# Kernel optimization log

Measured on AMD Instinct MI355X. Metric: run time of the kernel, lower is better.

## Reference

```python
import jax, jax.numpy as jnp
import numpy as np

N_ENTITIES = 500000
N_RELATIONS = 200
EMBED_DIM = 128
RELATION_DIM = 128  # must equal EMBED_DIM for the reshape in calculate_score
BATCH = 16384
KG_L2_LAMBDA = 1e-5


def _xavier_uniform(key, shape):
    fan_in, fan_out = shape[0], shape[1]
    limit = float(np.sqrt(6.0 / (fan_in + fan_out)))
    return jax.random.uniform(key, shape, jnp.float32, -limit, limit)


def setup_inputs() -> dict:
    key = jax.random.key(0)
    k1, k2, k3, k4, k5, k6 = jax.random.split(key, 6)
    entity_embed = _xavier_uniform(k1, (N_ENTITIES, EMBED_DIM))
    relation_embed = _xavier_uniform(k2, (N_RELATIONS, RELATION_DIM * EMBED_DIM))
    h = jax.random.randint(k3, (BATCH,), 0, N_ENTITIES, dtype=jnp.int64)
    r = jax.random.randint(k4, (BATCH,), 0, N_RELATIONS, dtype=jnp.int64)
    pos_t = jax.random.randint(k5, (BATCH,), 0, N_ENTITIES, dtype=jnp.int64)
    neg_t = jax.random.randint(k6, (BATCH,), 0, N_ENTITIES, dtype=jnp.int64)
    return {"h": h, "r": r, "pos_t": pos_t, "neg_t": neg_t,
            "entity_embed": entity_embed, "relation_embed": relation_embed}


def _l2_loss_mean(x):
    # mean over batch of sum(x^2, dim=1) / 2
    return jnp.mean(jnp.sum(x * x, axis=1) / 2.0)


def _score(h_e, t_e, r_mat):
    # r_mat: (B, relation_dim, embed_dim); tr = r @ t : (B, embed_dim)
    tr = jnp.einsum('bde,be->bd', r_mat, t_e)
    return -jnp.sum(h_e * tr, axis=-1)  # (B,)


def reference(h, r, pos_t, neg_t, entity_embed, relation_embed):
    r_embed = relation_embed[r]                     # (B, R*D)
    head_embed = entity_embed[h]                    # (B, D)
    tail_pos_embed = entity_embed[pos_t]            # (B, D)
    tail_neg_embed = entity_embed[neg_t]            # (B, D)
    r_mat = r_embed.reshape(-1, RELATION_DIM, EMBED_DIM)
    pos_score = _score(head_embed, tail_pos_embed, r_mat)
    neg_score = _score(head_embed, tail_neg_embed, r_mat)
    triplet_loss = jnp.mean(-jax.nn.log_sigmoid(neg_score - pos_score))
    l2_loss = (_l2_loss_mean(head_embed) + _l2_loss_mean(r_embed)
               + _l2_loss_mean(tail_pos_embed) + _l2_loss_mean(tail_neg_embed))
    return triplet_loss + KG_L2_LAMBDA * l2_loss
```

## Files before the change

### kernel.cpp

```cpp
#include <hip/hip_runtime.h>
#include <math.h>

#define BATCH 16384
#define EDIM 128
#define RD (EDIM * EDIM)
#define NREL 200
#define SPLIT 4
#define NBLK (NREL * SPLIT)
#define NTHR 256
#define QUARTER (BATCH / SPLIT)
#define NJ (QUARTER / NTHR)
#define EB 8
#define LISTCAP 256


__device__ __forceinline__ int load_idx(const void* p, int b, int is64) {
    if (is64) return (int)((const long long*)p)[b];
    return ((const int*)p)[b];
}

__global__ __launch_bounds__(NTHR) void rescal_kernel(
    const void* __restrict__ hI, const void* __restrict__ rI,
    const void* __restrict__ pI, const void* __restrict__ nI,
    const float* __restrict__ ent, const float* __restrict__ rel,
    float* __restrict__ csum) {
    const int t = threadIdx.x;
    const int bid0 = blockIdx.x;
    const int xcd = bid0 & 7;
    const int slot = bid0 >> 3;
    const int rid = xcd + 8 * (slot >> 2);
    const int qtr = slot & 3;
    const int lane = t & 63;
    const int wave = t >> 6;
    const int c2 = lane * 2;

    __shared__ unsigned short list[LISTCAP];
    __shared__ unsigned int wtj[NJ][4];
    __shared__ unsigned int um4[4];
    __shared__ float wsum[4];

    unsigned int o = ((const unsigned int*)hI)[2 * t + 1] |
                     ((const unsigned int*)rI)[2 * t + 1] |
                     ((const unsigned int*)pI)[2 * t + 1] |
                     ((const unsigned int*)nI)[2 * t + 1];
#pragma unroll
    for (int off = 32; off; off >>= 1) o |= __shfl_xor(o, off, 64);
    if (lane == 0) um4[wave] = o;
    __syncthreads();
    const int is64 = ((um4[0] | um4[1] | um4[2] | um4[3]) == 0u) ? 1 : 0;

    const int qbase = qtr * QUARTER;
    unsigned long long bal[NJ];
#pragma unroll
    for (int j = 0; j < NJ; ++j) {
        const int rr = load_idx(rI, qbase + j * NTHR + t, is64);
        bal[j] = __ballot(rr == rid);
        if (lane == 0) wtj[j][wave] = (unsigned int)__popcll(bal[j]);
    }
    __syncthreads();
    int cnt;
    {
        unsigned int run = 0;
        const unsigned long long ltmask = (lane == 63) ? ~0ull >> 1
                                                       : (1ull << lane) - 1ull;
#pragma unroll
        for (int j = 0; j < NJ; ++j) {
            unsigned int wpre = 0, tj = 0;
#pragma unroll
            for (int w = 0; w < 4; ++w) {
                const unsigned int v = wtj[j][w];
                tj += v;
                wpre += (w < wave) ? v : 0;
            }
            if ((bal[j] >> lane) & 1ull) {
                const unsigned int rank =
                    run + wpre + (unsigned int)__popcll(bal[j] & ltmask);
                if (rank < LISTCAP) list[rank] = (unsigned short)(j * NTHR + t);
            }
            run += tj;
        }
        cnt = (int)run;
        if (cnt > LISTCAP) cnt = LISTCAP;
    }
    __syncthreads();

    const int per_wave = (cnt + 3) >> 2;
    int lo = wave * per_wave;
    int hi = (wave + 1) * per_wave;
    if (lo > cnt) lo = cnt;
    if (hi > cnt) hi = cnt;

    const float* Rg = rel + (size_t)rid * RD;
    float lsum = 0.f;
    float r2w = 0.f;

    for (int e0 = lo; e0 < hi; e0 += EB) {
        int bidx[EB];
        const float* hrow[EB];
#pragma unroll
        for (int i = 0; i < EB; ++i) {
            int e = e0 + i;
            if (e >= hi) e = hi - 1;
            int b = qbase + (int)list[e];
            b = __builtin_amdgcn_readfirstlane(b);
            bidx[i] = b;
            int hix = load_idx(hI, b, is64);
            hix = __builtin_amdgcn_readfirstlane(hix);
            hrow[i] = ent + (size_t)hix * EDIM;
        }

        float2 acc[EB];
#pragma unroll
        for (int i = 0; i < EB; ++i) acc[i] = make_float2(0.f, 0.f);
        float r2p = 0.f;
#pragma unroll 4
        for (int db = 0; db < 32; ++db) {
            float4 hv0 = *(const float4*)(hrow[0] + db * 4);
            float4 hv1 = *(const float4*)(hrow[1] + db * 4);
            float4 hv2 = *(const float4*)(hrow[2] + db * 4);
            float4 hv3 = *(const float4*)(hrow[3] + db * 4);
            float4 hv4 = *(const float4*)(hrow[4] + db * 4);
            float4 hv5 = *(const float4*)(hrow[5] + db * 4);
            float4 hv6 = *(const float4*)(hrow[6] + db * 4);
            float4 hv7 = *(const float4*)(hrow[7] + db * 4);
#pragma unroll
            for (int jj = 0; jj < 4; ++jj) {
                const int d = db * 4 + jj;
                const float2 r2v = *(const float2*)(Rg + d * EDIM + c2);
                r2p = fmaf(r2v.x, r2v.x, fmaf(r2v.y, r2v.y, r2p));
                const float h0 = (jj == 0) ? hv0.x : (jj == 1) ? hv0.y : (jj == 2) ? hv0.z : hv0.w;
                const float h1 = (jj == 0) ? hv1.x : (jj == 1) ? hv1.y : (jj == 2) ? hv1.z : hv1.w;
                const float h2 = (jj == 0) ? hv2.x : (jj == 1) ? hv2.y : (jj == 2) ? hv2.z : hv2.w;
                const float h3 = (jj == 0) ? hv3.x : (jj == 1) ? hv3.y : (jj == 2) ? hv3.z : hv3.w;
                const float h4 = (jj == 0) ? hv4.x : (jj == 1) ? hv4.y : (jj == 2) ? hv4.z : hv4.w;
                const float h5 = (jj == 0) ? hv5.x : (jj == 1) ? hv5.y : (jj == 2) ? hv5.z : hv5.w;
                const float h6 = (jj == 0) ? hv6.x : (jj == 1) ? hv6.y : (jj == 2) ? hv6.z : hv6.w;
                const float h7 = (jj == 0) ? hv7.x : (jj == 1) ? hv7.y : (jj == 2) ? hv7.z : hv7.w;
                acc[0].x = fmaf(r2v.x, h0, acc[0].x); acc[0].y = fmaf(r2v.y, h0, acc[0].y);
                acc[1].x = fmaf(r2v.x, h1, acc[1].x); acc[1].y = fmaf(r2v.y, h1, acc[1].y);
                acc[2].x = fmaf(r2v.x, h2, acc[2].x); acc[2].y = fmaf(r2v.y, h2, acc[2].y);
                acc[3].x = fmaf(r2v.x, h3, acc[3].x); acc[3].y = fmaf(r2v.y, h3, acc[3].y);
                acc[4].x = fmaf(r2v.x, h4, acc[4].x); acc[4].y = fmaf(r2v.y, h4, acc[4].y);
                acc[5].x = fmaf(r2v.x, h5, acc[5].x); acc[5].y = fmaf(r2v.y, h5, acc[5].y);
                acc[6].x = fmaf(r2v.x, h6, acc[6].x); acc[6].y = fmaf(r2v.y, h6, acc[6].y);
                acc[7].x = fmaf(r2v.x, h7, acc[7].x); acc[7].y = fmaf(r2v.y, h7, acc[7].y);
            }
        }
#pragma unroll
        for (int off = 32; off; off >>= 1) r2p += __shfl_xor(r2p, off, 64);
        r2w = r2p;

#pragma unroll
        for (int i = 0; i < EB; ++i) {
            const int b = bidx[i];
            int pi = __builtin_amdgcn_readfirstlane(load_idx(pI, b, is64));
            int ni = __builtin_amdgcn_readfirstlane(load_idx(nI, b, is64));
            const float2 hv2 = *(const float2*)(hrow[i] + c2);
            const float2 tp2 = *(const float2*)(ent + (size_t)pi * EDIM + c2);
            const float2 tn2 = *(const float2*)(ent + (size_t)ni * EDIM + c2);
            float dp = acc[i].x * tp2.x + acc[i].y * tp2.y;
            float dn = acc[i].x * tn2.x + acc[i].y * tn2.y;
            float e2 = hv2.x * hv2.x + hv2.y * hv2.y + tp2.x * tp2.x + tp2.y * tp2.y +
                       tn2.x * tn2.x + tn2.y * tn2.y;
#pragma unroll
            for (int off = 32; off; off >>= 1) {
                dp += __shfl_xor(dp, off, 64);
                dn += __shfl_xor(dn, off, 64);
                e2 += __shfl_xor(e2, off, 64);
            }
            if (lane == 0 && (e0 + i) < hi) {
                const float x = dn - dp;
                const float spl = (x > 0.f) ? (x + log1pf(expf(-x))) : log1pf(expf(x));
                lsum += spl + 1e-5f * 0.5f * (e2 + r2w);
            }
        }
    }

    if (lane == 0) wsum[wave] = lsum;
    __syncthreads();
    if (t == 0) csum[bid0] = wsum[0] + wsum[1] + wsum[2] + wsum[3];
}

__global__ __launch_bounds__(NTHR) void reduce_kernel(const float* __restrict__ csum,
                                                      float* __restrict__ out) {
    const int t = threadIdx.x;
    float a = 0.f;
    for (int i = t; i < NBLK; i += NTHR) a += csum[i];
#pragma unroll
    for (int off = 32; off; off >>= 1) a += __shfl_down(a, off, 64);
    __shared__ float sm[4];
    if ((t & 63) == 0) sm[t >> 6] = a;
    __syncthreads();
    if (t == 0) out[0] = (sm[0] + sm[1] + sm[2] + sm[3]) * (1.0f / (float)BATCH);
}

extern "C" void kernel_launch(void* const* d_in, const int* in_sizes, int n_in,
                              void* d_out, int out_size, void* d_ws, size_t ws_size,
                              hipStream_t stream) {
    const void* h = d_in[0];
    const void* r = d_in[1];
    const void* pt = d_in[2];
    const void* nt = d_in[3];
    const float* ent = (const float*)d_in[4];
    const float* rel = (const float*)d_in[5];
    float* csum = (float*)d_ws;

    rescal_kernel<<<NBLK, NTHR, 0, stream>>>(h, r, pt, nt, ent, rel, csum);
    reduce_kernel<<<1, NTHR, 0, stream>>>(csum, (float*)d_out);
}
```

Measured before the change: 54.09 us.

## Split relation rows across waves and fuse final reduction via last-block atomic

Work inside a block is now split across the four waves by the d dimension of the relation matrix (32 rows per wave) instead of by batch entries. Each wave computes partial r@h products for groups of 16 entries, and the partials are summed through shared memory. This cuts each wave's relation-matrix reads to a quarter but adds two block barriers per group. The separate reduce kernel is replaced by a last-block-done atomic counter, reset by a memset, so one kernel launch is removed in exchange for a memset and fences.

```diff
diff --git a/kernel.cpp b/kernel.cpp
--- a/kernel.cpp
+++ b/kernel.cpp
@@ -10,7 +10,7 @@
 #define NTHR 256
 #define QUARTER (BATCH / SPLIT)
 #define NJ (QUARTER / NTHR)
-#define EB 8
+#define GE 16
 #define LISTCAP 256
 
 
@@ -23,7 +23,7 @@
     const void* __restrict__ hI, const void* __restrict__ rI,
     const void* __restrict__ pI, const void* __restrict__ nI,
     const float* __restrict__ ent, const float* __restrict__ rel,
-    float* __restrict__ csum) {
+    float* __restrict__ ws, float* __restrict__ out) {
     const int t = threadIdx.x;
     const int bid0 = blockIdx.x;
     const int xcd = bid0 & 7;
@@ -34,10 +34,12 @@
     const int wave = t >> 6;
     const int c2 = lane * 2;
 
+    __shared__ float uw[4][GE][EDIM];
     __shared__ unsigned short list[LISTCAP];
     __shared__ unsigned int wtj[NJ][4];
     __shared__ unsigned int um4[4];
-    __shared__ float wsum[4];
+    __shared__ float wred[4], wsum[4];
+    __shared__ int s_last;
 
     unsigned int o = ((const unsigned int*)hI)[2 * t + 1] |
                      ((const unsigned int*)rI)[2 * t + 1] |
@@ -84,23 +86,18 @@
     }
     __syncthreads();
 
-    const int per_wave = (cnt + 3) >> 2;
-    int lo = wave * per_wave;
-    int hi = (wave + 1) * per_wave;
-    if (lo > cnt) lo = cnt;
-    if (hi > cnt) hi = cnt;
-
     const float* Rg = rel + (size_t)rid * RD;
+    const int dlo = wave * 32;
     float lsum = 0.f;
-    float r2w = 0.f;
-
-    for (int e0 = lo; e0 < hi; e0 += EB) {
-        int bidx[EB];
-        const float* hrow[EB];
-#pragma unroll
-        for (int i = 0; i < EB; ++i) {
-            int e = e0 + i;
-            if (e >= hi) e = hi - 1;
+    float r2sum = 0.f;
+
+    for (int g0 = 0; g0 < cnt; g0 += GE) {
+        int bidx[GE];
+        const float* hrow[GE];
+#pragma unroll
+        for (int i = 0; i < GE; ++i) {
+            int e = g0 + i;
+            if (e >= cnt) e = cnt - 1;
             int b = qbase + (int)list[e];
             b = __builtin_amdgcn_readfirstlane(b);
             bidx[i] = b;
@@ -109,57 +106,52 @@
             hrow[i] = ent + (size_t)hix * EDIM;
         }
 
-        float2 acc[EB];
-#pragma unroll
-        for (int i = 0; i < EB; ++i) acc[i] = make_float2(0.f, 0.f);
+        float2 acc[GE];
+#pragma unroll
+        for (int i = 0; i < GE; ++i) acc[i] = make_float2(0.f, 0.f);
         float r2p = 0.f;
 #pragma unroll 4
-        for (int db = 0; db < 32; ++db) {
-            float4 hv0 = *(const float4*)(hrow[0] + db * 4);
-            float4 hv1 = *(const float4*)(hrow[1] + db * 4);
-            float4 hv2 = *(const float4*)(hrow[2] + db * 4);
-            float4 hv3 = *(const float4*)(hrow[3] + db * 4);
-            float4 hv4 = *(const float4*)(hrow[4] + db * 4);
-            float4 hv5 = *(const float4*)(hrow[5] + db * 4);
-            float4 hv6 = *(const float4*)(hrow[6] + db * 4);
-            float4 hv7 = *(const float4*)(hrow[7] + db * 4);
-#pragma unroll
-            for (int jj = 0; jj < 4; ++jj) {
-                const int d = db * 4 + jj;
-                const float2 r2v = *(const float2*)(Rg + d * EDIM + c2);
-                r2p = fmaf(r2v.x, r2v.x, fmaf(r2v.y, r2v.y, r2p));
-                const float h0 = (jj == 0) ? hv0.x : (jj == 1) ? hv0.y : (jj == 2) ? hv0.z : hv0.w;
-                const float h1 = (jj == 0) ? hv1.x : (jj == 1) ? hv1.y : (jj == 2) ? hv1.z : hv1.w;
-                const float h2 = (jj == 0) ? hv2.x : (jj == 1) ? hv2.y : (jj == 2) ? hv2.z : hv2.w;
-                const float h3 = (jj == 0) ? hv3.x : (jj == 1) ? hv3.y : (jj == 2) ? hv3.z : hv3.w;
-                const float h4 = (jj == 0) ? hv4.x : (jj == 1) ? hv4.y : (jj == 2) ? hv4.z : hv4.w;
-                const float h5 = (jj == 0) ? hv5.x : (jj == 1) ? hv5.y : (jj == 2) ? hv5.z : hv5.w;
-                const float h6 = (jj == 0) ? hv6.x : (jj == 1) ? hv6.y : (jj == 2) ? hv6.z : hv6.w;
-                const float h7 = (jj == 0) ? hv7.x : (jj == 1) ? hv7.y : (jj == 2) ? hv7.z : hv7.w;
-                acc[0].x = fmaf(r2v.x, h0, acc[0].x); acc[0].y = fmaf(r2v.y, h0, acc[0].y);
-                acc[1].x = fmaf(r2v.x, h1, acc[1].x); acc[1].y = fmaf(r2v.y, h1, acc[1].y);
-                acc[2].x = fmaf(r2v.x, h2, acc[2].x); acc[2].y = fmaf(r2v.y, h2, acc[2].y);
-                acc[3].x = fmaf(r2v.x, h3, acc[3].x); acc[3].y = fmaf(r2v.y, h3, acc[3].y);
-                acc[4].x = fmaf(r2v.x, h4, acc[4].x); acc[4].y = fmaf(r2v.y, h4, acc[4].y);
-                acc[5].x = fmaf(r2v.x, h5, acc[5].x); acc[5].y = fmaf(r2v.y, h5, acc[5].y);
-                acc[6].x = fmaf(r2v.x, h6, acc[6].x); acc[6].y = fmaf(r2v.y, h6, acc[6].y);
-                acc[7].x = fmaf(r2v.x, h7, acc[7].x); acc[7].y = fmaf(r2v.y, h7, acc[7].y);
-            }
-        }
-#pragma unroll
-        for (int off = 32; off; off >>= 1) r2p += __shfl_xor(r2p, off, 64);
-        r2w = r2p;
-
-#pragma unroll
-        for (int i = 0; i < EB; ++i) {
+        for (int db = 0; db < 16; ++db) {
+            const int d0 = dlo + db * 2;
+            const float2 ra = *(const float2*)(Rg + d0 * EDIM + c2);
+            const float2 rb = *(const float2*)(Rg + (d0 + 1) * EDIM + c2);
+            r2p = fmaf(ra.x, ra.x, fmaf(ra.y, ra.y, fmaf(rb.x, rb.x, fmaf(rb.y, rb.y, r2p))));
+#pragma unroll
+            for (int i = 0; i < GE; ++i) {
+                const float2 hd = *(const float2*)(hrow[i] + d0);
+                acc[i].x = fmaf(ra.x, hd.x, acc[i].x);
+                acc[i].y = fmaf(ra.y, hd.x, acc[i].y);
+                acc[i].x = fmaf(rb.x, hd.y, acc[i].x);
+                acc[i].y = fmaf(rb.y, hd.y, acc[i].y);
+            }
+        }
+#pragma unroll
+        for (int i = 0; i < GE; ++i) *(float2*)&uw[wave][i][c2] = acc[i];
+        if (g0 == 0) {
+#pragma unroll
+            for (int off = 32; off; off >>= 1) r2p += __shfl_xor(r2p, off, 64);
+            if (lane == 0) wred[wave] = r2p;
+        }
+        __syncthreads();
+        if (g0 == 0) r2sum = wred[0] + wred[1] + wred[2] + wred[3];
+
+#pragma unroll
+        for (int q = 0; q < 4; ++q) {
+            const int i = wave * 4 + q;
+            const float2 v0 = *(const float2*)&uw[0][i][c2];
+            const float2 v1 = *(const float2*)&uw[1][i][c2];
+            const float2 v2 = *(const float2*)&uw[2][i][c2];
+            const float2 v3 = *(const float2*)&uw[3][i][c2];
+            const float ux = v0.x + v1.x + v2.x + v3.x;
+            const float uy = v0.y + v1.y + v2.y + v3.y;
             const int b = bidx[i];
-            int pi = __builtin_amdgcn_readfirstlane(load_idx(pI, b, is64));
-            int ni = __builtin_amdgcn_readfirstlane(load_idx(nI, b, is64));
+            const int pi = __builtin_amdgcn_readfirstlane(load_idx(pI, b, is64));
+            const int ni = __builtin_amdgcn_readfirstlane(load_idx(nI, b, is64));
             const float2 hv2 = *(const float2*)(hrow[i] + c2);
             const float2 tp2 = *(const float2*)(ent + (size_t)pi * EDIM + c2);
             const float2 tn2 = *(const float2*)(ent + (size_t)ni * EDIM + c2);
-            float dp = acc[i].x * tp2.x + acc[i].y * tp2.y;
-            float dn = acc[i].x * tn2.x + acc[i].y * tn2.y;
+            float dp = ux * tp2.x + uy * tp2.y;
+            float dn = ux * tn2.x + uy * tn2.y;
             float e2 = hv2.x * hv2.x + hv2.y * hv2.y + tp2.x * tp2.x + tp2.y * tp2.y +
                        tn2.x * tn2.x + tn2.y * tn2.y;
 #pragma unroll
@@ -168,30 +160,36 @@
                 dn += __shfl_xor(dn, off, 64);
                 e2 += __shfl_xor(e2, off, 64);
             }
-            if (lane == 0 && (e0 + i) < hi) {
+            if (lane == 0 && (g0 + i) < cnt) {
                 const float x = dn - dp;
                 const float spl = (x > 0.f) ? (x + log1pf(expf(-x))) : log1pf(expf(x));
-                lsum += spl + 1e-5f * 0.5f * (e2 + r2w);
-            }
-        }
+                lsum += spl + 1e-5f * 0.5f * (e2 + r2sum);
+            }
+        }
+        __syncthreads();
     }
 
     if (lane == 0) wsum[wave] = lsum;
     __syncthreads();
-    if (t == 0) csum[bid0] = wsum[0] + wsum[1] + wsum[2] + wsum[3];
-}
-
-__global__ __launch_bounds__(NTHR) void reduce_kernel(const float* __restrict__ csum,
-                                                      float* __restrict__ out) {
-    const int t = threadIdx.x;
-    float a = 0.f;
-    for (int i = t; i < NBLK; i += NTHR) a += csum[i];
-#pragma unroll
-    for (int off = 32; off; off >>= 1) a += __shfl_down(a, off, 64);
-    __shared__ float sm[4];
-    if ((t & 63) == 0) sm[t >> 6] = a;
-    __syncthreads();
-    if (t == 0) out[0] = (sm[0] + sm[1] + sm[2] + sm[3]) * (1.0f / (float)BATCH);
+    if (t == 0) {
+        ws[bid0] = wsum[0] + wsum[1] + wsum[2] + wsum[3];
+        __threadfence();
+        unsigned int old = atomicAdd((unsigned int*)(ws + 1024), 1u);
+        s_last = (old == (unsigned int)(NBLK - 1)) ? 1 : 0;
+    }
+    __syncthreads();
+    if (s_last) {
+        __threadfence();
+        float a = 0.f;
+        for (int i = t; i < NBLK; i += NTHR)
+            a += __hip_atomic_load(&ws[i], __ATOMIC_ACQUIRE, __HIP_MEMORY_SCOPE_AGENT);
+#pragma unroll
+        for (int off = 32; off; off >>= 1) a += __shfl_down(a, off, 64);
+        if (lane == 0) wsum[wave] = a;
+        __syncthreads();
+        if (t == 0)
+            out[0] = (wsum[0] + wsum[1] + wsum[2] + wsum[3]) * (1.0f / (float)BATCH);
+    }
 }
 
 extern "C" void kernel_launch(void* const* d_in, const int* in_sizes, int n_in,
@@ -203,8 +201,9 @@
     const void* nt = d_in[3];
     const float* ent = (const float*)d_in[4];
     const float* rel = (const float*)d_in[5];
-    float* csum = (float*)d_ws;
-
-    rescal_kernel<<<NBLK, NTHR, 0, stream>>>(h, r, pt, nt, ent, rel, csum);
-    reduce_kernel<<<1, NTHR, 0, stream>>>(csum, (float*)d_out);
+
+    hipMemsetAsync((void*)((char*)d_ws + 1024 * sizeof(float)), 0,
+                   sizeof(unsigned int), stream);
+    rescal_kernel<<<NBLK, NTHR, 0, stream>>>(h, r, pt, nt, ent, rel,
+                                             (float*)d_ws, (float*)d_out);
 }
```

New measurement: 126.6 us. +134.1%, slower.

## Split each relation across eight blocks and fuse final reduction via last-block atomic

Applied to the files above, without the earlier changes.

Doubles the per-relation batch split from 4 to 8 blocks (1600 blocks total) with a smaller entity batch of 4 and a smaller per-block list, which adds parallelism and lowers register pressure. The tail-embedding loads are hoisted ahead of the matvec loop so their latency overlaps it. The separate reduce kernel is removed: a last-block-done atomic counter now does the final sum inside the main kernel, at the cost of an extra memset launch. Each relation matrix is now re-read by twice as many blocks, and a smaller LISTCAP raises the risk of truncation if a relation's count exceeds 128 per piece.

```diff
diff --git a/kernel.cpp b/kernel.cpp
--- a/kernel.cpp
+++ b/kernel.cpp
@@ -5,13 +5,13 @@
 #define EDIM 128
 #define RD (EDIM * EDIM)
 #define NREL 200
-#define SPLIT 4
+#define SPLIT 8
 #define NBLK (NREL * SPLIT)
 #define NTHR 256
-#define QUARTER (BATCH / SPLIT)
-#define NJ (QUARTER / NTHR)
-#define EB 8
-#define LISTCAP 256
+#define PIECE (BATCH / SPLIT)
+#define NJ (PIECE / NTHR)
+#define EB 4
+#define LISTCAP 128
 
 
 __device__ __forceinline__ int load_idx(const void* p, int b, int is64) {
@@ -23,13 +23,13 @@
     const void* __restrict__ hI, const void* __restrict__ rI,
     const void* __restrict__ pI, const void* __restrict__ nI,
     const float* __restrict__ ent, const float* __restrict__ rel,
-    float* __restrict__ csum) {
+    float* __restrict__ ws, float* __restrict__ out) {
     const int t = threadIdx.x;
     const int bid0 = blockIdx.x;
     const int xcd = bid0 & 7;
     const int slot = bid0 >> 3;
-    const int rid = xcd + 8 * (slot >> 2);
-    const int qtr = slot & 3;
+    const int rid = xcd + 8 * (slot >> 3);
+    const int piece = slot & 7;
     const int lane = t & 63;
     const int wave = t >> 6;
     const int c2 = lane * 2;
@@ -38,6 +38,7 @@
     __shared__ unsigned int wtj[NJ][4];
     __shared__ unsigned int um4[4];
     __shared__ float wsum[4];
+    __shared__ int s_last;
 
     unsigned int o = ((const unsigned int*)hI)[2 * t + 1] |
                      ((const unsigned int*)rI)[2 * t + 1] |
@@ -49,7 +50,7 @@
     __syncthreads();
     const int is64 = ((um4[0] | um4[1] | um4[2] | um4[3]) == 0u) ? 1 : 0;
 
-    const int qbase = qtr * QUARTER;
+    const int qbase = piece * PIECE;
     unsigned long long bal[NJ];
 #pragma unroll
     for (int j = 0; j < NJ; ++j) {
@@ -92,7 +93,6 @@
 
     const float* Rg = rel + (size_t)rid * RD;
     float lsum = 0.f;
-    float r2w = 0.f;
 
     for (int e0 = lo; e0 < hi; e0 += EB) {
         int bidx[EB];
@@ -109,59 +109,53 @@
             hrow[i] = ent + (size_t)hix * EDIM;
         }
 
+        float2 tpv[EB], tnv[EB], hvv[EB];
+#pragma unroll
+        for (int i = 0; i < EB; ++i) {
+            const int b = bidx[i];
+            const int pi = __builtin_amdgcn_readfirstlane(load_idx(pI, b, is64));
+            const int ni = __builtin_amdgcn_readfirstlane(load_idx(nI, b, is64));
+            tpv[i] = *(const float2*)(ent + (size_t)pi * EDIM + c2);
+            tnv[i] = *(const float2*)(ent + (size_t)ni * EDIM + c2);
+            hvv[i] = *(const float2*)(hrow[i] + c2);
+        }
+
         float2 acc[EB];
 #pragma unroll
         for (int i = 0; i < EB; ++i) acc[i] = make_float2(0.f, 0.f);
         float r2p = 0.f;
 #pragma unroll 4
         for (int db = 0; db < 32; ++db) {
-            float4 hv0 = *(const float4*)(hrow[0] + db * 4);
-            float4 hv1 = *(const float4*)(hrow[1] + db * 4);
-            float4 hv2 = *(const float4*)(hrow[2] + db * 4);
-            float4 hv3 = *(const float4*)(hrow[3] + db * 4);
-            float4 hv4 = *(const float4*)(hrow[4] + db * 4);
-            float4 hv5 = *(const float4*)(hrow[5] + db * 4);
-            float4 hv6 = *(const float4*)(hrow[6] + db * 4);
-            float4 hv7 = *(const float4*)(hrow[7] + db * 4);
+            const float4 hv0 = *(const float4*)(hrow[0] + db * 4);
+            const float4 hv1 = *(const float4*)(hrow[1] + db * 4);
+            const float4 hv2 = *(const float4*)(hrow[2] + db * 4);
+            const float4 hv3 = *(const float4*)(hrow[3] + db * 4);
 #pragma unroll
             for (int jj = 0; jj < 4; ++jj) {
                 const int d = db * 4 + jj;
-                const float2 r2v = *(const float2*)(Rg + d * EDIM + c2);
-                r2p = fmaf(r2v.x, r2v.x, fmaf(r2v.y, r2v.y, r2p));
+                const float2 rv = *(const float2*)(Rg + d * EDIM + c2);
+                r2p = fmaf(rv.x, rv.x, fmaf(rv.y, rv.y, r2p));
                 const float h0 = (jj == 0) ? hv0.x : (jj == 1) ? hv0.y : (jj == 2) ? hv0.z : hv0.w;
                 const float h1 = (jj == 0) ? hv1.x : (jj == 1) ? hv1.y : (jj == 2) ? hv1.z : hv1.w;
                 const float h2 = (jj == 0) ? hv2.x : (jj == 1) ? hv2.y : (jj == 2) ? hv2.z : hv2.w;
                 const float h3 = (jj == 0) ? hv3.x : (jj == 1) ? hv3.y : (jj == 2) ? hv3.z : hv3.w;
-                const float h4 = (jj == 0) ? hv4.x : (jj == 1) ? hv4.y : (jj == 2) ? hv4.z : hv4.w;
-                const float h5 = (jj == 0) ? hv5.x : (jj == 1) ? hv5.y : (jj == 2) ? hv5.z : hv5.w;
-                const float h6 = (jj == 0) ? hv6.x : (jj == 1) ? hv6.y : (jj == 2) ? hv6.z : hv6.w;
-                const float h7 = (jj == 0) ? hv7.x : (jj == 1) ? hv7.y : (jj == 2) ? hv7.z : hv7.w;
-                acc[0].x = fmaf(r2v.x, h0, acc[0].x); acc[0].y = fmaf(r2v.y, h0, acc[0].y);
-                acc[1].x = fmaf(r2v.x, h1, acc[1].x); acc[1].y = fmaf(r2v.y, h1, acc[1].y);
-                acc[2].x = fmaf(r2v.x, h2, acc[2].x); acc[2].y = fmaf(r2v.y, h2, acc[2].y);
-                acc[3].x = fmaf(r2v.x, h3, acc[3].x); acc[3].y = fmaf(r2v.y, h3, acc[3].y);
-                acc[4].x = fmaf(r2v.x, h4, acc[4].x); acc[4].y = fmaf(r2v.y, h4, acc[4].y);
-                acc[5].x = fmaf(r2v.x, h5, acc[5].x); acc[5].y = fmaf(r2v.y, h5, acc[5].y);
-                acc[6].x = fmaf(r2v.x, h6, acc[6].x); acc[6].y = fmaf(r2v.y, h6, acc[6].y);
-                acc[7].x = fmaf(r2v.x, h7, acc[7].x); acc[7].y = fmaf(r2v.y, h7, acc[7].y);
+                acc[0].x = fmaf(rv.x, h0, acc[0].x); acc[0].y = fmaf(rv.y, h0, acc[0].y);
+                acc[1].x = fmaf(rv.x, h1, acc[1].x); acc[1].y = fmaf(rv.y, h1, acc[1].y);
+                acc[2].x = fmaf(rv.x, h2, acc[2].x); acc[2].y = fmaf(rv.y, h2, acc[2].y);
+                acc[3].x = fmaf(rv.x, h3, acc[3].x); acc[3].y = fmaf(rv.y, h3, acc[3].y);
             }
         }
 #pragma unroll
         for (int off = 32; off; off >>= 1) r2p += __shfl_xor(r2p, off, 64);
-        r2w = r2p;
+        const float r2w = r2p;
 
 #pragma unroll
         for (int i = 0; i < EB; ++i) {
-            const int b = bidx[i];
-            int pi = __builtin_amdgcn_readfirstlane(load_idx(pI, b, is64));
-            int ni = __builtin_amdgcn_readfirstlane(load_idx(nI, b, is64));
-            const float2 hv2 = *(const float2*)(hrow[i] + c2);
-            const float2 tp2 = *(const float2*)(ent + (size_t)pi * EDIM + c2);
-            const float2 tn2 = *(const float2*)(ent + (size_t)ni * EDIM + c2);
-            float dp = acc[i].x * tp2.x + acc[i].y * tp2.y;
-            float dn = acc[i].x * tn2.x + acc[i].y * tn2.y;
-            float e2 = hv2.x * hv2.x + hv2.y * hv2.y + tp2.x * tp2.x + tp2.y * tp2.y +
-                       tn2.x * tn2.x + tn2.y * tn2.y;
+            float dp = acc[i].x * tpv[i].x + acc[i].y * tpv[i].y;
+            float dn = acc[i].x * tnv[i].x + acc[i].y * tnv[i].y;
+            float e2 = hvv[i].x * hvv[i].x + hvv[i].y * hvv[i].y +
+                       tpv[i].x * tpv[i].x + tpv[i].y * tpv[i].y +
+                       tnv[i].x * tnv[i].x + tnv[i].y * tnv[i].y;
 #pragma unroll
             for (int off = 32; off; off >>= 1) {
                 dp += __shfl_xor(dp, off, 64);
@@ -178,20 +172,25 @@
 
     if (lane == 0) wsum[wave] = lsum;
     __syncthreads();
-    if (t == 0) csum[bid0] = wsum[0] + wsum[1] + wsum[2] + wsum[3];
-}
-
-__global__ __launch_bounds__(NTHR) void reduce_kernel(const float* __restrict__ csum,
-                                                      float* __restrict__ out) {
-    const int t = threadIdx.x;
-    float a = 0.f;
-    for (int i = t; i < NBLK; i += NTHR) a += csum[i];
-#pragma unroll
-    for (int off = 32; off; off >>= 1) a += __shfl_down(a, off, 64);
-    __shared__ float sm[4];
-    if ((t & 63) == 0) sm[t >> 6] = a;
-    __syncthreads();
-    if (t == 0) out[0] = (sm[0] + sm[1] + sm[2] + sm[3]) * (1.0f / (float)BATCH);
+    if (t == 0) {
+        ws[bid0] = wsum[0] + wsum[1] + wsum[2] + wsum[3];
+        __threadfence();
+        unsigned int old = atomicAdd((unsigned int*)(ws + 2048), 1u);
+        s_last = (old == (unsigned int)(NBLK - 1)) ? 1 : 0;
+    }
+    __syncthreads();
+    if (s_last) {
+        __threadfence();
+        float a = 0.f;
+        for (int i = t; i < NBLK; i += NTHR)
+            a += __hip_atomic_load(&ws[i], __ATOMIC_ACQUIRE, __HIP_MEMORY_SCOPE_AGENT);
+#pragma unroll
+        for (int off = 32; off; off >>= 1) a += __shfl_down(a, off, 64);
+        if (lane == 0) wsum[wave] = a;
+        __syncthreads();
+        if (t == 0)
+            out[0] = (wsum[0] + wsum[1] + wsum[2] + wsum[3]) * (1.0f / (float)BATCH);
+    }
 }
 
 extern "C" void kernel_launch(void* const* d_in, const int* in_sizes, int n_in,
@@ -203,8 +202,9 @@
     const void* nt = d_in[3];
     const float* ent = (const float*)d_in[4];
     const float* rel = (const float*)d_in[5];
-    float* csum = (float*)d_ws;
-
-    rescal_kernel<<<NBLK, NTHR, 0, stream>>>(h, r, pt, nt, ent, rel, csum);
-    reduce_kernel<<<1, NTHR, 0, stream>>>(csum, (float*)d_out);
+
+    hipMemsetAsync((void*)((char*)d_ws + 2048 * sizeof(float)), 0,
+                   sizeof(unsigned int), stream);
+    rescal_kernel<<<NBLK, NTHR, 0, stream>>>(h, r, pt, nt, ent, rel,
+                                             (float*)d_ws, (float*)d_out);
 }
```

Measured after the change: 80.65 us. 1.49x slower.

## Stage relation matrix in LDS, widen blocks to 512 threads, precompute its norm

Applied to the files above, without the earlier changes.

Each block now copies its 64KB relation matrix into shared memory once and computes its squared norm during that copy. Previously every entity batch re-read the matrix from global memory and recomputed the norm. The block grows to 8 waves with 4 entities per wave batch instead of 8, so more waves share the staged matrix. The 64KB LDS per block limits how many blocks fit on a CU, and the up-front copy adds latency before compute starts.

```diff
diff --git a/kernel.cpp b/kernel.cpp
--- a/kernel.cpp
+++ b/kernel.cpp
@@ -7,10 +7,10 @@
 #define NREL 200
 #define SPLIT 4
 #define NBLK (NREL * SPLIT)
-#define NTHR 256
+#define NTHR 512
 #define QUARTER (BATCH / SPLIT)
 #define NJ (QUARTER / NTHR)
-#define EB 8
+#define EBW 4
 #define LISTCAP 256
 
 
@@ -19,7 +19,7 @@
     return ((const int*)p)[b];
 }
 
-__global__ __launch_bounds__(NTHR) void rescal_kernel(
+__global__ __launch_bounds__(NTHR, 4) void rescal_kernel(
     const void* __restrict__ hI, const void* __restrict__ rI,
     const void* __restrict__ pI, const void* __restrict__ nI,
     const float* __restrict__ ent, const float* __restrict__ rel,
@@ -34,20 +34,36 @@
     const int wave = t >> 6;
     const int c2 = lane * 2;
 
+    __shared__ __attribute__((aligned(16))) float Rl[RD];
     __shared__ unsigned short list[LISTCAP];
-    __shared__ unsigned int wtj[NJ][4];
-    __shared__ unsigned int um4[4];
-    __shared__ float wsum[4];
-
-    unsigned int o = ((const unsigned int*)hI)[2 * t + 1] |
-                     ((const unsigned int*)rI)[2 * t + 1] |
-                     ((const unsigned int*)pI)[2 * t + 1] |
-                     ((const unsigned int*)nI)[2 * t + 1];
+    __shared__ unsigned int wtj[NJ][8];
+    __shared__ unsigned int um8[8];
+    __shared__ float rsq[8], wsum[8];
+
+    unsigned int o = 0u;
+    if (t < 256) {
+        o = ((const unsigned int*)hI)[2 * t + 1] | ((const unsigned int*)rI)[2 * t + 1] |
+            ((const unsigned int*)pI)[2 * t + 1] | ((const unsigned int*)nI)[2 * t + 1];
+    }
 #pragma unroll
     for (int off = 32; off; off >>= 1) o |= __shfl_xor(o, off, 64);
-    if (lane == 0) um4[wave] = o;
-    __syncthreads();
-    const int is64 = ((um4[0] | um4[1] | um4[2] | um4[3]) == 0u) ? 1 : 0;
+    if (lane == 0) um8[wave] = o;
+    __syncthreads();
+    const int is64 = ((um8[0] | um8[1] | um8[2] | um8[3] |
+                       um8[4] | um8[5] | um8[6] | um8[7]) == 0u) ? 1 : 0;
+
+    const float* Rg = rel + (size_t)rid * RD;
+    float r2p = 0.f;
+#pragma unroll
+    for (int it = 0; it < 8; ++it) {
+        const int idx = it * (NTHR * 4) + t * 4;
+        const float4 v = *(const float4*)(Rg + idx);
+        *(float4*)&Rl[idx] = v;
+        r2p = fmaf(v.x, v.x, fmaf(v.y, v.y, fmaf(v.z, v.z, fmaf(v.w, v.w, r2p))));
+    }
+#pragma unroll
+    for (int off = 32; off; off >>= 1) r2p += __shfl_xor(r2p, off, 64);
+    if (lane == 0) rsq[wave] = r2p;
 
     const int qbase = qtr * QUARTER;
     unsigned long long bal[NJ];
@@ -58,6 +74,7 @@
         if (lane == 0) wtj[j][wave] = (unsigned int)__popcll(bal[j]);
     }
     __syncthreads();
+
     int cnt;
     {
         unsigned int run = 0;
@@ -67,7 +84,7 @@
         for (int j = 0; j < NJ; ++j) {
             unsigned int wpre = 0, tj = 0;
 #pragma unroll
-            for (int w = 0; w < 4; ++w) {
+            for (int w = 0; w < 8; ++w) {
                 const unsigned int v = wtj[j][w];
                 tj += v;
                 wpre += (w < wave) ? v : 0;
@@ -84,21 +101,22 @@
     }
     __syncthreads();
 
-    const int per_wave = (cnt + 3) >> 2;
+    const float r2sum = rsq[0] + rsq[1] + rsq[2] + rsq[3] +
+                        rsq[4] + rsq[5] + rsq[6] + rsq[7];
+
+    const int per_wave = (cnt + 7) >> 3;
     int lo = wave * per_wave;
     int hi = (wave + 1) * per_wave;
     if (lo > cnt) lo = cnt;
     if (hi > cnt) hi = cnt;
 
-    const float* Rg = rel + (size_t)rid * RD;
     float lsum = 0.f;
-    float r2w = 0.f;
-
-    for (int e0 = lo; e0 < hi; e0 += EB) {
-        int bidx[EB];
-        const float* hrow[EB];
-#pragma unroll
-        for (int i = 0; i < EB; ++i) {
+
+    for (int e0 = lo; e0 < hi; e0 += EBW) {
+        int bidx[EBW];
+        const float* hrow[EBW];
+#pragma unroll
+        for (int i = 0; i < EBW; ++i) {
             int e = e0 + i;
             if (e >= hi) e = hi - 1;
             int b = qbase + (int)list[e];
@@ -109,52 +127,35 @@
             hrow[i] = ent + (size_t)hix * EDIM;
         }
 
-        float2 acc[EB];
-#pragma unroll
-        for (int i = 0; i < EB; ++i) acc[i] = make_float2(0.f, 0.f);
-        float r2p = 0.f;
+        float2 acc[EBW];
+#pragma unroll
+        for (int i = 0; i < EBW; ++i) acc[i] = make_float2(0.f, 0.f);
 #pragma unroll 4
         for (int db = 0; db < 32; ++db) {
-            float4 hv0 = *(const float4*)(hrow[0] + db * 4);
-            float4 hv1 = *(const float4*)(hrow[1] + db * 4);
-            float4 hv2 = *(const float4*)(hrow[2] + db * 4);
-            float4 hv3 = *(const float4*)(hrow[3] + db * 4);
-            float4 hv4 = *(const float4*)(hrow[4] + db * 4);
-            float4 hv5 = *(const float4*)(hrow[5] + db * 4);
-            float4 hv6 = *(const float4*)(hrow[6] + db * 4);
-            float4 hv7 = *(const float4*)(hrow[7] + db * 4);
+            const float4 hv0 = *(const float4*)(hrow[0] + db * 4);
+            const float4 hv1 = *(const float4*)(hrow[1] + db * 4);
+            const float4 hv2 = *(const float4*)(hrow[2] + db * 4);
+            const float4 hv3 = *(const float4*)(hrow[3] + db * 4);
 #pragma unroll
             for (int jj = 0; jj < 4; ++jj) {
                 const int d = db * 4 + jj;
-                const float2 r2v = *(const float2*)(Rg + d * EDIM + c2);
-                r2p = fmaf(r2v.x, r2v.x, fmaf(r2v.y, r2v.y, r2p));
+                const float2 rv = *(const float2*)&Rl[d * EDIM + c2];
                 const float h0 = (jj == 0) ? hv0.x : (jj == 1) ? hv0.y : (jj == 2) ? hv0.z : hv0.w;
                 const float h1 = (jj == 0) ? hv1.x : (jj == 1) ? hv1.y : (jj == 2) ? hv1.z : hv1.w;
                 const float h2 = (jj == 0) ? hv2.x : (jj == 1) ? hv2.y : (jj == 2) ? hv2.z : hv2.w;
                 const float h3 = (jj == 0) ? hv3.x : (jj == 1) ? hv3.y : (jj == 2) ? hv3.z : hv3.w;
-                const float h4 = (jj == 0) ? hv4.x : (jj == 1) ? hv4.y : (jj == 2) ? hv4.z : hv4.w;
-                const float h5 = (jj == 0) ? hv5.x : (jj == 1) ? hv5.y : (jj == 2) ? hv5.z : hv5.w;
-                const float h6 = (jj == 0) ? hv6.x : (jj == 1) ? hv6.y : (jj == 2) ? hv6.z : hv6.w;
-                const float h7 = (jj == 0) ? hv7.x : (jj == 1) ? hv7.y : (jj == 2) ? hv7.z : hv7.w;
-                acc[0].x = fmaf(r2v.x, h0, acc[0].x); acc[0].y = fmaf(r2v.y, h0, acc[0].y);
-                acc[1].x = fmaf(r2v.x, h1, acc[1].x); acc[1].y = fmaf(r2v.y, h1, acc[1].y);
-                acc[2].x = fmaf(r2v.x, h2, acc[2].x); acc[2].y = fmaf(r2v.y, h2, acc[2].y);
-                acc[3].x = fmaf(r2v.x, h3, acc[3].x); acc[3].y = fmaf(r2v.y, h3, acc[3].y);
-                acc[4].x = fmaf(r2v.x, h4, acc[4].x); acc[4].y = fmaf(r2v.y, h4, acc[4].y);
-                acc[5].x = fmaf(r2v.x, h5, acc[5].x); acc[5].y = fmaf(r2v.y, h5, acc[5].y);
-                acc[6].x = fmaf(r2v.x, h6, acc[6].x); acc[6].y = fmaf(r2v.y, h6, acc[6].y);
-                acc[7].x = fmaf(r2v.x, h7, acc[7].x); acc[7].y = fmaf(r2v.y, h7, acc[7].y);
-            }
-        }
-#pragma unroll
-        for (int off = 32; off; off >>= 1) r2p += __shfl_xor(r2p, off, 64);
-        r2w = r2p;
-
-#pragma unroll
-        for (int i = 0; i < EB; ++i) {
+                acc[0].x = fmaf(rv.x, h0, acc[0].x); acc[0].y = fmaf(rv.y, h0, acc[0].y);
+                acc[1].x = fmaf(rv.x, h1, acc[1].x); acc[1].y = fmaf(rv.y, h1, acc[1].y);
+                acc[2].x = fmaf(rv.x, h2, acc[2].x); acc[2].y = fmaf(rv.y, h2, acc[2].y);
+                acc[3].x = fmaf(rv.x, h3, acc[3].x); acc[3].y = fmaf(rv.y, h3, acc[3].y);
+            }
+        }
+
+#pragma unroll
+        for (int i = 0; i < EBW; ++i) {
             const int b = bidx[i];
-            int pi = __builtin_amdgcn_readfirstlane(load_idx(pI, b, is64));
-            int ni = __builtin_amdgcn_readfirstlane(load_idx(nI, b, is64));
+            const int pi = __builtin_amdgcn_readfirstlane(load_idx(pI, b, is64));
+            const int ni = __builtin_amdgcn_readfirstlane(load_idx(nI, b, is64));
             const float2 hv2 = *(const float2*)(hrow[i] + c2);
             const float2 tp2 = *(const float2*)(ent + (size_t)pi * EDIM + c2);
             const float2 tn2 = *(const float2*)(ent + (size_t)ni * EDIM + c2);
@@ -171,21 +172,24 @@
             if (lane == 0 && (e0 + i) < hi) {
                 const float x = dn - dp;
                 const float spl = (x > 0.f) ? (x + log1pf(expf(-x))) : log1pf(expf(x));
-                lsum += spl + 1e-5f * 0.5f * (e2 + r2w);
+                lsum += spl + 1e-5f * 0.5f * (e2 + r2sum);
             }
         }
     }
 
     if (lane == 0) wsum[wave] = lsum;
     __syncthreads();
-    if (t == 0) csum[bid0] = wsum[0] + wsum[1] + wsum[2] + wsum[3];
-}
-
-__global__ __launch_bounds__(NTHR) void reduce_kernel(const float* __restrict__ csum,
-                                                      float* __restrict__ out) {
+    if (t == 0) {
+        csum[bid0] = wsum[0] + wsum[1] + wsum[2] + wsum[3] +
+                     wsum[4] + wsum[5] + wsum[6] + wsum[7];
+    }
+}
+
+__global__ __launch_bounds__(256) void reduce_kernel(const float* __restrict__ csum,
+                                                     float* __restrict__ out) {
     const int t = threadIdx.x;
     float a = 0.f;
-    for (int i = t; i < NBLK; i += NTHR) a += csum[i];
+    for (int i = t; i < NBLK; i += 256) a += csum[i];
 #pragma unroll
     for (int off = 32; off; off >>= 1) a += __shfl_down(a, off, 64);
     __shared__ float sm[4];
@@ -206,5 +210,5 @@
     float* csum = (float*)d_ws;
 
     rescal_kernel<<<NBLK, NTHR, 0, stream>>>(h, r, pt, nt, ent, rel, csum);
-    reduce_kernel<<<1, NTHR, 0, stream>>>(csum, (float*)d_out);
-}
+    reduce_kernel<<<1, 256, 0, stream>>>(csum, (float*)d_out);
+}
```

Measured after the change: 47.24 us (median of 3 runs). 12.7% less time.
